# Optimization experiments

Measured on AMD Instinct MI355X. Metric: run time of the kernel, lower is better.

The kernel has to match this reference:

```python
import jax, jax.numpy as jnp
import numpy as np

N = 8192      # total nodes = B * NPG
D = 512       # in_dim = hidden_dim = out_dim
E = 131072    # edges
B = 16        # graphs (selected_idx batch)
NPG = 512     # nodes per graph
S = 128       # selected nodes per graph
L = 3         # conv layers
EPS = 1e-5


def setup_inputs() -> dict:
    key = jax.random.key(0)
    ks = jax.random.split(key, 16)
    scale = 0.02
    return {
        "x": jax.random.normal(ks[0], (N, D), dtype=jnp.float32),
        "edge_index": jax.random.randint(ks[1], (2, E), 0, N),
        "selected_idx": jax.random.randint(ks[2], (B, S), 0, NPG),
        "edge_label": jax.random.randint(ks[3], (E,), 0, 4),
        # per-layer EdgeConv MLP params (stacked over L layers)
        "conv_W1": jax.random.normal(ks[4], (L, 2 * D, D), dtype=jnp.float32) * scale,
        "conv_b1": jnp.full((L, D), 0.01, dtype=jnp.float32),
        "conv_W2": jax.random.normal(ks[5], (L, D, D), dtype=jnp.float32) * scale,
        "conv_b2": jnp.full((L, D), 0.01, dtype=jnp.float32),
        # shared layer norms
        "ln1_g": jnp.ones((D,), dtype=jnp.float32),
        "ln1_b": jnp.zeros((D,), dtype=jnp.float32),
        "ln2_g": jnp.ones((D,), dtype=jnp.float32),
        "ln2_b": jnp.zeros((D,), dtype=jnp.float32),
        # final FFN
        "ffn_W1": jax.random.normal(ks[6], (D, D), dtype=jnp.float32) * scale,
        "ffn_b1": jnp.full((D,), 0.01, dtype=jnp.float32),
        "ffn_W2": jax.random.normal(ks[7], (D, D), dtype=jnp.float32) * scale,
        "ffn_b2": jnp.full((D,), 0.01, dtype=jnp.float32),
    }


def _layer_norm(x, g, b):
    mu = jnp.mean(x, axis=-1, keepdims=True)
    var = jnp.mean(jnp.square(x - mu), axis=-1, keepdims=True)
    return (x - mu) * jax.lax.rsqrt(var + EPS) * g + b


def reference(x, edge_index, selected_idx, edge_label,
              conv_W1, conv_b1, conv_W2, conv_b2,
              ln1_g, ln1_b, ln2_g, ln2_b,
              ffn_W1, ffn_b1, ffn_W2, ffn_b2):
    src = edge_index[0]  # x_j source nodes
    dst = edge_index[1]  # x_i target nodes (aggregation index)
    for l in range(L):
        residual = x
        h = _layer_norm(x, ln1_g, ln1_b)
        hi = h[dst]                                   # [E, D]
        hj = h[src]                                   # [E, D]
        ef = jnp.concatenate([hi, hj - hi], axis=1)   # [E, 2D]
        m = jnp.maximum(ef @ conv_W1[l] + conv_b1[l], 0.0) @ conv_W2[l] + conv_b2[l]
        agg = jax.ops.segment_max(m, dst, num_segments=N)  # max-aggregate [N, D]
        agg = jnp.where(jnp.isfinite(agg), agg, 0.0)       # nodes w/o in-edges -> 0
        x = jnp.maximum(agg, 0.0) + residual
    residual = x
    h = _layer_norm(x, ln2_g, ln2_b)
    y = jnp.maximum(h @ ffn_W1 + ffn_b1, 0.0) @ ffn_W2 + ffn_b2
    x = y + residual
    x = x.reshape(B, NPG, D)
    idx = jnp.broadcast_to(selected_idx[:, :, None], (B, S, D))
    return jnp.take_along_axis(x, idx, axis=1)  # [B, S, D]
```

## Files before the change

### kernel.cpp

```cpp
#include <hip/hip_runtime.h>
#include <stdint.h>

#define NN 8192
#define DD 512
#define EE 131072
#define BBATCH 16
#define NPG 512
#define SSEL 128
#define LL 3

typedef unsigned short u16;
typedef __bf16 bf16x8 __attribute__((ext_vector_type(8)));
typedef float f32x4 __attribute__((ext_vector_type(4)));
typedef u16 u16x8 __attribute__((ext_vector_type(8)));

__device__ __forceinline__ float bf2f(u16 u) {
    union { unsigned i; float f; } v; v.i = ((unsigned)u) << 16; return v.f;
}
__device__ __forceinline__ u16 f2bf(float f) {
    union { unsigned i; float f; } v; v.f = f;
    unsigned i = v.i;
    return (u16)((i + 0x7FFFu + ((i >> 16) & 1u)) >> 16);
}

__device__ __forceinline__ void async_cp16(const u16* g, u16* l) {
    __builtin_amdgcn_global_load_lds(
        (const __attribute__((address_space(1))) unsigned int*)g,
        (__attribute__((address_space(3))) unsigned int*)l, 16, 0, 0);
}

__global__ __launch_bounds__(64) void ln_fused(const float* __restrict__ xin,
                                               float* __restrict__ agg_io,
                                               float* __restrict__ xout,
                                               const float* __restrict__ g,
                                               const float* __restrict__ b,
                                               u16* __restrict__ h, int doAdd) {
    int row = blockIdx.x;
    int lane = threadIdx.x;
    const f32x4* x4 = (const f32x4*)(xin + (size_t)row * DD);
    f32x4 p = x4[lane * 2], q = x4[lane * 2 + 1];
    if (doAdd) {
        const f32x4* a4 = (const f32x4*)(agg_io + (size_t)row * DD);
        f32x4 pa = a4[lane * 2], qa = a4[lane * 2 + 1];
        #pragma unroll
        for (int i = 0; i < 4; ++i) { p[i] += pa[i]; q[i] += qa[i]; }
    }
    if (agg_io) {
        f32x4 z;
        #pragma unroll
        for (int i = 0; i < 4; ++i) z[i] = 0.f;
        f32x4* a4 = (f32x4*)(agg_io + (size_t)row * DD);
        a4[lane * 2] = z;
        a4[lane * 2 + 1] = z;
    }
    f32x4* xo = (f32x4*)(xout + (size_t)row * DD);
    xo[lane * 2] = p;
    xo[lane * 2 + 1] = q;
    float v[8];
    v[0] = p[0]; v[1] = p[1]; v[2] = p[2]; v[3] = p[3];
    v[4] = q[0]; v[5] = q[1]; v[6] = q[2]; v[7] = q[3];
    float s = 0.f, sq = 0.f;
    #pragma unroll
    for (int i = 0; i < 8; ++i) { s += v[i]; sq += v[i] * v[i]; }
    #pragma unroll
    for (int o = 32; o >= 1; o >>= 1) { s += __shfl_xor(s, o); sq += __shfl_xor(sq, o); }
    float mu = s * (1.f / DD);
    float var = sq * (1.f / DD) - mu * mu;
    float rs = rsqrtf(var + 1e-5f);
    int kb = lane * 8;
    u16x8 o8;
    #pragma unroll
    for (int i = 0; i < 8; ++i) o8[i] = f2bf((v[i] - mu) * rs * g[kb + i] + b[kb + i]);
    *(u16x8*)(h + (size_t)row * DD + kb) = o8;
}

__global__ void hist_kernel(const int* __restrict__ dst, int* __restrict__ cnt) {
    int e = blockIdx.x * 256 + threadIdx.x;
    if (e < EE) atomicAdd(&cnt[dst[e]], 1);
}

__global__ __launch_bounds__(1024) void scan_kernel(const int* __restrict__ cnt,
                                                    int* __restrict__ off,
                                                    int* __restrict__ cur) {
    __shared__ int part[1024];
    int t = threadIdx.x;
    int base = t * 8;
    int loc[8]; int s = 0;
    #pragma unroll
    for (int i = 0; i < 8; ++i) { loc[i] = s; s += cnt[base + i]; }
    part[t] = s;
    __syncthreads();
    for (int o = 1; o < 1024; o <<= 1) {
        int v = part[t];
        int u = (t >= o) ? part[t - o] : 0;
        __syncthreads();
        part[t] = v + u;
        __syncthreads();
    }
    int bx = (t > 0) ? part[t - 1] : 0;
    #pragma unroll
    for (int i = 0; i < 8; ++i) { off[base + i] = bx + loc[i]; cur[base + i] = bx + loc[i]; }
    if (t == 0) off[NN] = part[1023];
}

__global__ void scatter_kernel(const int* __restrict__ src, const int* __restrict__ dst,
                               int* __restrict__ cur, int* __restrict__ ssrc,
                               int* __restrict__ sdst) {
    int e = blockIdx.x * 256 + threadIdx.x;
    if (e < EE) {
        int d = dst[e];
        int p = atomicAdd(&cur[d], 1);
        ssrc[p] = src[e];
        sdst[p] = d;
    }
}

__global__ __launch_bounds__(256) void cvt_t_kernel(const float* __restrict__ src,
                                                    u16* __restrict__ dstp, int K,
                                                    int Nn) {
    __shared__ u16 tile[32][33];
    int bk = blockIdx.x * 32, bn = blockIdx.y * 32;
    int tx = threadIdx.x & 31, ty = threadIdx.x >> 5;
    #pragma unroll
    for (int r = 0; r < 32; r += 8)
        tile[ty + r][tx] = f2bf(src[(size_t)(bk + ty + r) * Nn + bn + tx]);
    __syncthreads();
    #pragma unroll
    for (int r = 0; r < 32; r += 8)
        dstp[(size_t)(bn + ty + r) * K + bk + tx] = tile[tx][ty + r];
}

__global__ __launch_bounds__(256) void cvt_w1_kernel(const float* __restrict__ W1,
                                                     u16* __restrict__ dstp) {
    __shared__ u16 tile[32][33];
    int bk = blockIdx.x * 32, bn = blockIdx.y * 32;
    int tx = threadIdx.x & 31, ty = threadIdx.x >> 5;
    #pragma unroll
    for (int r = 0; r < 32; r += 8) {
        int k = bk + ty + r, n = bn + tx;
        float v = (n < 512) ? (W1[(size_t)k * 512 + n] - W1[(size_t)(k + 512) * 512 + n])
                            : W1[(size_t)(k + 512) * 512 + (n - 512)];
        tile[ty + r][tx] = f2bf(v);
    }
    __syncthreads();
    #pragma unroll
    for (int r = 0; r < 32; r += 8)
        dstp[(size_t)(bn + ty + r) * 512 + bk + tx] = tile[tx][ty + r];
}

template <int EMODE>
__global__ __launch_bounds__(256) void gemm_async(
    const u16* __restrict__ A, const u16* __restrict__ BT,
    const float* __restrict__ bias, const float* __restrict__ resid,
    void* __restrict__ Cout, int K, int ldc) {
    __shared__ u16 lA[128 * 64];
    __shared__ u16 lB[128 * 64];
    const int tid = threadIdx.x;
    const int lane = tid & 63, wave = tid >> 6;
    const int wm = wave & 1, wn = wave >> 1;
    const int quad = lane >> 4, lm = lane & 15;
    const int tileM = blockIdx.x, tileN = blockIdx.y;

    const int g = (lane & 7) ^ (lane >> 3);
    const u16* ap[4];
    const u16* bp[4];
    u16* lad[4];
    u16* lbd[4];
    #pragma unroll
    for (int j = 0; j < 4; ++j) {
        int seg = wave * 4 + j;
        int rA = tileM * 128 + seg * 8 + (lane >> 3);
        int rB = tileN * 128 + seg * 8 + (lane >> 3);
        ap[j] = A + (size_t)rA * K + g * 8;
        bp[j] = BT + (size_t)rB * K + g * 8;
        lad[j] = lA + seg * 512;
        lbd[j] = lB + seg * 512;
    }

    f32x4 acc[4][4];
    #pragma unroll
    for (int mt = 0; mt < 4; ++mt)
        #pragma unroll
        for (int nt = 0; nt < 4; ++nt)
            #pragma unroll
            for (int j = 0; j < 4; ++j) acc[mt][nt][j] = 0.f;

    for (int kb = 0; kb < K; kb += 64) {
        #pragma unroll
        for (int j = 0; j < 4; ++j) {
            async_cp16(ap[j], lad[j]);
            async_cp16(bp[j], lbd[j]);
            ap[j] += 64;
            bp[j] += 64;
        }
        __syncthreads();
        #pragma unroll
        for (int kk = 0; kk < 64; kk += 32) {
            bf16x8 af[4], bfr[4];
            int gbase = (kk >> 3) + quad;
            #pragma unroll
            for (int mt = 0; mt < 4; ++mt) {
                int row = wm * 64 + mt * 16 + lm;
                af[mt] = *(const bf16x8*)(lA + row * 64 + ((gbase ^ (row & 7)) << 3));
            }
            #pragma unroll
            for (int nt = 0; nt < 4; ++nt) {
                int row = wn * 64 + nt * 16 + lm;
                bfr[nt] = *(const bf16x8*)(lB + row * 64 + ((gbase ^ (row & 7)) << 3));
            }
            #pragma unroll
            for (int mt = 0; mt < 4; ++mt)
                #pragma unroll
                for (int nt = 0; nt < 4; ++nt)
                    acc[mt][nt] = __builtin_amdgcn_mfma_f32_16x16x32_bf16(
                        af[mt], bfr[nt], acc[mt][nt], 0, 0, 0);
        }
        __syncthreads();
    }
    #pragma unroll
    for (int mt = 0; mt < 4; ++mt) {
        #pragma unroll
        for (int nt = 0; nt < 4; ++nt) {
            int col = tileN * 128 + wn * 64 + nt * 16 + lm;
            float bv;
            if (EMODE == 2) bv = 0.f;
            else if (EMODE == 3) bv = (col < 512) ? bias[col] : 0.f;
            else bv = bias[col];
            #pragma unroll
            for (int j = 0; j < 4; ++j) {
                int grow = tileM * 128 + wm * 64 + mt * 16 + quad * 4 + j;
                float v = acc[mt][nt][j] + bv;
                if (EMODE == 0) {
                    ((u16*)Cout)[(size_t)grow * ldc + col] = f2bf(fmaxf(v, 0.f));
                } else if (EMODE == 1) {
                    ((float*)Cout)[(size_t)grow * ldc + col] =
                        v + resid[(size_t)grow * ldc + col];
                } else {
                    ((u16*)Cout)[(size_t)grow * ldc + col] = f2bf(v);
                }
            }
        }
    }
}

__global__ __launch_bounds__(512, 4) void gemm_edge(
    const u16* __restrict__ P, const int* __restrict__ ssrc,
    const int* __restrict__ sdst, const u16* __restrict__ W2T,
    const float* __restrict__ b2, float* __restrict__ agg) {
    __shared__ u16 smem[128 * 64 + 256 * 64];
    __shared__ int nid_l[128];
    u16* lA = smem;
    u16* lB = smem + 128 * 64;
    const int tid = threadIdx.x;
    const int lane = tid & 63, wave = tid >> 6;
    const int wm = wave & 1, wn = wave >> 1;
    const int quad = lane >> 4, lm = lane & 15;
    const int tileN = blockIdx.x;
    const int ebase = blockIdx.y * 128;

    if (tid < 128) nid_l[tid] = sdst[ebase + tid];

    const int g = (lane & 7) ^ (lane >> 3);
    int aoff[2], boff[2];
    u16* lout[2];
    #pragma unroll
    for (int j = 0; j < 2; ++j) {
        int seg = wave * 2 + j;
        int row = seg * 8 + (lane >> 3);
        int dn = sdst[ebase + row];
        int sn = ssrc[ebase + row];
        aoff[j] = dn * 1024 + g * 8;
        boff[j] = sn * 1024 + 512 + g * 8;
        lout[j] = lA + seg * 512 + lane * 8;
    }
    int woff[4];
    u16* lbd[4];
    #pragma unroll
    for (int j = 0; j < 4; ++j) {
        int seg = wave * 4 + j;
        int row = tileN * 256 + seg * 8 + (lane >> 3);
        woff[j] = row * 512 + g * 8;
        lbd[j] = lB + seg * 512;
    }

    f32x4 acc[4][4];
    #pragma unroll
    for (int mt = 0; mt < 4; ++mt)
        #pragma unroll
        for (int nt = 0; nt < 4; ++nt)
            #pragma unroll
            for (int j = 0; j < 4; ++j) acc[mt][nt][j] = 0.f;

    for (int kb = 0; kb < 512; kb += 64) {
        u16x8 ga[2], gb[2];
        #pragma unroll
        for (int j = 0; j < 2; ++j) {
            ga[j] = *(const u16x8*)(P + aoff[j] + kb);
            gb[j] = *(const u16x8*)(P + boff[j] + kb);
        }
        #pragma unroll
        for (int j = 0; j < 4; ++j) async_cp16(W2T + woff[j] + kb, lbd[j]);
        #pragma unroll
        for (int j = 0; j < 2; ++j) {
            union { u16x8 v; unsigned w[4]; } ua, ub;
            ua.v = ga[j];
            ub.v = gb[j];
            unsigned o[4];
            #pragma unroll
            for (int q = 0; q < 4; ++q) {
                float a0 = __uint_as_float(ua.w[q] << 16);
                float a1 = __uint_as_float(ua.w[q] & 0xffff0000u);
                float c0 = __uint_as_float(ub.w[q] << 16);
                float c1 = __uint_as_float(ub.w[q] & 0xffff0000u);
                float s0 = fmaxf(a0 + c0, 0.f);
                float s1 = fmaxf(a1 + c1, 0.f);
                unsigned r0 = __float_as_uint(s0) + 0x8000u;
                unsigned r1 = __float_as_uint(s1) + 0x8000u;
                o[q] = (r0 >> 16) | (r1 & 0xffff0000u);
            }
            *(uint4*)lout[j] = make_uint4(o[0], o[1], o[2], o[3]);
        }
        __syncthreads();
        #pragma unroll
        for (int kk = 0; kk < 64; kk += 32) {
            bf16x8 af[4], bfr[4];
            int gbase = (kk >> 3) + quad;
            #pragma unroll
            for (int mt = 0; mt < 4; ++mt) {
                int row = wm * 64 + mt * 16 + lm;
                af[mt] = *(const bf16x8*)(lA + row * 64 + ((gbase ^ (row & 7)) << 3));
            }
            #pragma unroll
            for (int nt = 0; nt < 4; ++nt) {
                int row = wn * 64 + nt * 16 + lm;
                bfr[nt] = *(const bf16x8*)(lB + row * 64 + ((gbase ^ (row & 7)) << 3));
            }
            #pragma unroll
            for (int mt = 0; mt < 4; ++mt)
                #pragma unroll
                for (int nt = 0; nt < 4; ++nt)
                    acc[mt][nt] = __builtin_amdgcn_mfma_f32_16x16x32_bf16(
                        af[mt], bfr[nt], acc[mt][nt], 0, 0, 0);
        }
        __syncthreads();
    }

    u16* cbuf = smem;
    for (int p = 0; p < 2; ++p) {
        if (wm == p) {
            #pragma unroll
            for (int nt = 0; nt < 4; ++nt) {
                int lcol = wn * 64 + nt * 16 + lm;
                float bv = b2[tileN * 256 + lcol];
                #pragma unroll
                for (int mt = 0; mt < 4; ++mt) {
                    #pragma unroll
                    for (int j2 = 0; j2 < 4; ++j2) {
                        int row = mt * 16 + quad * 4 + j2;
                        cbuf[row * 264 + lcol] = f2bf(fmaxf(acc[mt][nt][j2] + bv, 0.f));
                    }
                }
            }
        }
        __syncthreads();
        {
            int lcol = tid & 255;
            int gcol = tileN * 256 + lcol;
            int r0 = (tid >> 8) * 32;
            int gr0 = p * 64 + r0;
            int cur = nid_l[gr0];
            float run = bf2f(cbuf[r0 * 264 + lcol]);
            for (int r = 1; r < 32; ++r) {
                int nd = nid_l[gr0 + r];
                float v = bf2f(cbuf[(r0 + r) * 264 + lcol]);
                if (nd != cur) {
                    atomicMax((unsigned int*)&agg[(size_t)cur * DD + gcol],
                              __float_as_uint(run));
                    cur = nd;
                    run = v;
                } else {
                    run = fmaxf(run, v);
                }
            }
            atomicMax((unsigned int*)&agg[(size_t)cur * DD + gcol],
                      __float_as_uint(run));
        }
        __syncthreads();
    }
}

__global__ __launch_bounds__(128) void gather_fused(const float* __restrict__ x,
                                                    const float* __restrict__ agg,
                                                    const int* __restrict__ sel,
                                                    float* __restrict__ xs) {
    int i = blockIdx.x;
    int b = i >> 7;
    int r = b * NPG + sel[i];
    const f32x4* srcp = (const f32x4*)(x + (size_t)r * DD);
    const f32x4* aggp = (const f32x4*)(agg + (size_t)r * DD);
    f32x4 v = srcp[threadIdx.x];
    f32x4 a = aggp[threadIdx.x];
    #pragma unroll
    for (int j = 0; j < 4; ++j) v[j] += a[j];
    ((f32x4*)(xs + (size_t)i * DD))[threadIdx.x] = v;
}

extern "C" void kernel_launch(void* const* d_in, const int* in_sizes, int n_in,
                              void* d_out, int out_size, void* d_ws, size_t ws_size,
                              hipStream_t stream) {
    const float* x_in = (const float*)d_in[0];
    const int* ei = (const int*)d_in[1];
    const int* sel = (const int*)d_in[2];
    const float* W1 = (const float*)d_in[4];
    const float* b1 = (const float*)d_in[5];
    const float* W2 = (const float*)d_in[6];
    const float* b2 = (const float*)d_in[7];
    const float* g1 = (const float*)d_in[8];
    const float* be1 = (const float*)d_in[9];
    const float* g2 = (const float*)d_in[10];
    const float* be2 = (const float*)d_in[11];
    const float* fW1 = (const float*)d_in[12];
    const float* fb1 = (const float*)d_in[13];
    const float* fW2 = (const float*)d_in[14];
    const float* fb2 = (const float*)d_in[15];
    float* out = (float*)d_out;

    char* w = (char*)d_ws;
    size_t off = 0;
    auto alloc = [&](size_t bytes) -> char* {
        char* p = w + off;
        off += (bytes + 255) & ~(size_t)255;
        return p;
    };
    float* xbuf = (float*)alloc((size_t)NN * DD * 4);
    float* agg  = (float*)alloc((size_t)NN * DD * 4);
    u16* h      = (u16*)alloc((size_t)NN * DD * 2);
    u16* P      = (u16*)alloc((size_t)NN * 1024 * 2);
    u16* W1T    = (u16*)alloc((size_t)LL * 1024 * DD * 2);
    u16* W2T    = (u16*)alloc((size_t)LL * DD * DD * 2);
    u16* FW1T   = (u16*)alloc((size_t)DD * DD * 2);
    u16* FW2T   = (u16*)alloc((size_t)DD * DD * 2);
    int* cnt    = (int*)alloc((size_t)NN * 4);
    int* offs   = (int*)alloc((size_t)(NN + 1) * 4);
    int* cur    = (int*)alloc((size_t)NN * 4);
    int* ssrc   = (int*)alloc((size_t)EE * 4);
    int* sdst   = (int*)alloc((size_t)EE * 4);
    float* xs   = (float*)alloc((size_t)BBATCH * SSEL * DD * 4);
    u16* hs     = (u16*)alloc((size_t)BBATCH * SSEL * DD * 2);
    u16* uu     = (u16*)alloc((size_t)BBATCH * SSEL * DD * 2);

    const int* esrc = ei;
    const int* edst = ei + EE;

    hipMemsetAsync(cnt, 0, (size_t)NN * 4, stream);
    hist_kernel<<<EE / 256, 256, 0, stream>>>(edst, cnt);
    scan_kernel<<<1, 1024, 0, stream>>>(cnt, offs, cur);
    scatter_kernel<<<EE / 256, 256, 0, stream>>>(esrc, edst, cur, ssrc, sdst);

    for (int l = 0; l < LL; ++l) {
        cvt_w1_kernel<<<dim3(16, 32), 256, 0, stream>>>(
            W1 + (size_t)l * 1024 * DD, W1T + (size_t)l * 1024 * DD);
        cvt_t_kernel<<<dim3(16, 16), 256, 0, stream>>>(
            W2 + (size_t)l * DD * DD, W2T + (size_t)l * DD * DD, DD, DD);
    }
    cvt_t_kernel<<<dim3(16, 16), 256, 0, stream>>>(fW1, FW1T, DD, DD);
    cvt_t_kernel<<<dim3(16, 16), 256, 0, stream>>>(fW2, FW2T, DD, DD);

    for (int l = 0; l < LL; ++l) {
        ln_fused<<<NN, 64, 0, stream>>>(l == 0 ? x_in : xbuf, agg, xbuf, g1, be1, h,
                                        l > 0 ? 1 : 0);
        {
            dim3 grid(NN / 128, 1024 / 128);
            gemm_async<3><<<grid, 256, 0, stream>>>(
                h, W1T + (size_t)l * 1024 * DD, b1 + (size_t)l * DD, nullptr, P, DD,
                1024);
        }
        gemm_edge<<<dim3(2, EE / 128), 512, 0, stream>>>(
            P, ssrc, sdst, W2T + (size_t)l * DD * DD, b2 + (size_t)l * DD, agg);
    }

    gather_fused<<<BBATCH * SSEL, 128, 0, stream>>>(xbuf, agg, sel, xs);
    ln_fused<<<BBATCH * SSEL, 64, 0, stream>>>(xs, nullptr, xs, g2, be2, hs, 0);
    dim3 gridf(BBATCH * SSEL / 128, DD / 128);
    gemm_async<0><<<gridf, 256, 0, stream>>>(hs, FW1T, fb1, nullptr, uu, DD, DD);
    gemm_async<1><<<gridf, 256, 0, stream>>>(uu, FW2T, fb2, xs, out, DD, DD);
}
```

Before: 620.2 us.

## Batch weight conversions, pack four LN rows per block, use packed bf16 convert

Merges the per-layer weight transpose/convert launches into two launches, using blockIdx.z to index layers or jobs. Changes the layernorm kernel to process four rows per 256-thread block instead of one row per 64-thread block. Replaces the manual round-and-pack in the edge GEMM's relu prologue with a packed bf16 conversion builtin and vector max. Together these aim to cut launch overhead and ALU work. The packed builtin rounds to nearest-even, whereas the old code rounded half-up, so results may differ slightly.

```diff
diff --git a/kernel.cpp b/kernel.cpp
--- a/kernel.cpp
+++ b/kernel.cpp
@@ -12,6 +12,7 @@
 typedef unsigned short u16;
 typedef __bf16 bf16x8 __attribute__((ext_vector_type(8)));
 typedef float f32x4 __attribute__((ext_vector_type(4)));
+typedef float f32x2 __attribute__((ext_vector_type(2)));
 typedef u16 u16x8 __attribute__((ext_vector_type(8)));
 
 __device__ __forceinline__ float bf2f(u16 u) {
@@ -23,20 +24,35 @@
     return (u16)((i + 0x7FFFu + ((i >> 16) & 1u)) >> 16);
 }
 
+__device__ __forceinline__ unsigned pk_bf16(float s0, float s1) {
+#if __has_builtin(__builtin_amdgcn_cvt_pk_bf16_f32)
+    typedef __bf16 bf16x2 __attribute__((ext_vector_type(2)));
+    union { bf16x2 v; unsigned u; } r;
+    r.v = __builtin_amdgcn_cvt_pk_bf16_f32(s0, s1);
+    return r.u;
+#else
+    unsigned r0 = __float_as_uint(s0);
+    r0 = (r0 + 0x7FFFu + ((r0 >> 16) & 1u)) >> 16;
+    unsigned r1 = __float_as_uint(s1);
+    r1 = (r1 + 0x7FFFu + ((r1 >> 16) & 1u)) & 0xffff0000u;
+    return r0 | r1;
+#endif
+}
+
 __device__ __forceinline__ void async_cp16(const u16* g, u16* l) {
     __builtin_amdgcn_global_load_lds(
         (const __attribute__((address_space(1))) unsigned int*)g,
         (__attribute__((address_space(3))) unsigned int*)l, 16, 0, 0);
 }
 
-__global__ __launch_bounds__(64) void ln_fused(const float* __restrict__ xin,
-                                               float* __restrict__ agg_io,
-                                               float* __restrict__ xout,
-                                               const float* __restrict__ g,
-                                               const float* __restrict__ b,
-                                               u16* __restrict__ h, int doAdd) {
-    int row = blockIdx.x;
-    int lane = threadIdx.x;
+__global__ __launch_bounds__(256) void ln_fused(const float* __restrict__ xin,
+                                                float* __restrict__ agg_io,
+                                                float* __restrict__ xout,
+                                                const float* __restrict__ g,
+                                                const float* __restrict__ b,
+                                                u16* __restrict__ h, int doAdd) {
+    int row = blockIdx.x * 4 + (threadIdx.x >> 6);
+    int lane = threadIdx.x & 63;
     const f32x4* x4 = (const f32x4*)(xin + (size_t)row * DD);
     f32x4 p = x4[lane * 2], q = x4[lane * 2 + 1];
     if (doAdd) {
@@ -115,24 +131,30 @@
     }
 }
 
-__global__ __launch_bounds__(256) void cvt_t_kernel(const float* __restrict__ src,
-                                                    u16* __restrict__ dstp, int K,
-                                                    int Nn) {
+struct CvtJobs {
+    const float* s[5];
+    u16* d[5];
+};
+__global__ __launch_bounds__(256) void cvt_t5_kernel(CvtJobs jobs) {
     __shared__ u16 tile[32][33];
+    const float* src = jobs.s[blockIdx.z];
+    u16* dstp = jobs.d[blockIdx.z];
     int bk = blockIdx.x * 32, bn = blockIdx.y * 32;
     int tx = threadIdx.x & 31, ty = threadIdx.x >> 5;
     #pragma unroll
     for (int r = 0; r < 32; r += 8)
-        tile[ty + r][tx] = f2bf(src[(size_t)(bk + ty + r) * Nn + bn + tx]);
+        tile[ty + r][tx] = f2bf(src[(size_t)(bk + ty + r) * 512 + bn + tx]);
     __syncthreads();
     #pragma unroll
     for (int r = 0; r < 32; r += 8)
-        dstp[(size_t)(bn + ty + r) * K + bk + tx] = tile[tx][ty + r];
-}
-
-__global__ __launch_bounds__(256) void cvt_w1_kernel(const float* __restrict__ W1,
-                                                     u16* __restrict__ dstp) {
+        dstp[(size_t)(bn + ty + r) * 512 + bk + tx] = tile[tx][ty + r];
+}
+
+__global__ __launch_bounds__(256) void cvt_w1_kernel(const float* __restrict__ W1g,
+                                                     u16* __restrict__ dstg) {
     __shared__ u16 tile[32][33];
+    const float* W1 = W1g + (size_t)blockIdx.z * 1024 * 512;
+    u16* dstp = dstg + (size_t)blockIdx.z * 1024 * 512;
     int bk = blockIdx.x * 32, bn = blockIdx.y * 32;
     int tx = threadIdx.x & 31, ty = threadIdx.x >> 5;
     #pragma unroll
@@ -308,15 +330,20 @@
             unsigned o[4];
             #pragma unroll
             for (int q = 0; q < 4; ++q) {
-                float a0 = __uint_as_float(ua.w[q] << 16);
-                float a1 = __uint_as_float(ua.w[q] & 0xffff0000u);
-                float c0 = __uint_as_float(ub.w[q] << 16);
-                float c1 = __uint_as_float(ub.w[q] & 0xffff0000u);
-                float s0 = fmaxf(a0 + c0, 0.f);
-                float s1 = fmaxf(a1 + c1, 0.f);
-                unsigned r0 = __float_as_uint(s0) + 0x8000u;
-                unsigned r1 = __float_as_uint(s1) + 0x8000u;
-                o[q] = (r0 >> 16) | (r1 & 0xffff0000u);
+                f32x2 a, c;
+                a[0] = __uint_as_float(ua.w[q] << 16);
+                a[1] = __uint_as_float(ua.w[q] & 0xffff0000u);
+                c[0] = __uint_as_float(ub.w[q] << 16);
+                c[1] = __uint_as_float(ub.w[q] & 0xffff0000u);
+                f32x2 s = a + c;
+#if __has_builtin(__builtin_elementwise_max)
+                f32x2 z; z[0] = 0.f; z[1] = 0.f;
+                s = __builtin_elementwise_max(s, z);
+#else
+                s[0] = fmaxf(s[0], 0.f);
+                s[1] = fmaxf(s[1], 0.f);
+#endif
+                o[q] = pk_bf16(s[0], s[1]);
             }
             *(uint4*)lout[j] = make_uint4(o[0], o[1], o[2], o[3]);
         }
@@ -457,18 +484,25 @@
     scan_kernel<<<1, 1024, 0, stream>>>(cnt, offs, cur);
     scatter_kernel<<<EE / 256, 256, 0, stream>>>(esrc, edst, cur, ssrc, sdst);
 
+    cvt_w1_kernel<<<dim3(16, 32, LL), 256, 0, stream>>>(W1, W1T);
+    {
+        CvtJobs jobs;
+        jobs.s[0] = W2;
+        jobs.s[1] = W2 + (size_t)DD * DD;
+        jobs.s[2] = W2 + (size_t)2 * DD * DD;
+        jobs.s[3] = fW1;
+        jobs.s[4] = fW2;
+        jobs.d[0] = W2T;
+        jobs.d[1] = W2T + (size_t)DD * DD;
+        jobs.d[2] = W2T + (size_t)2 * DD * DD;
+        jobs.d[3] = FW1T;
+        jobs.d[4] = FW2T;
+        cvt_t5_kernel<<<dim3(16, 16, 5), 256, 0, stream>>>(jobs);
+    }
+
     for (int l = 0; l < LL; ++l) {
-        cvt_w1_kernel<<<dim3(16, 32), 256, 0, stream>>>(
-            W1 + (size_t)l * 1024 * DD, W1T + (size_t)l * 1024 * DD);
-        cvt_t_kernel<<<dim3(16, 16), 256, 0, stream>>>(
-            W2 + (size_t)l * DD * DD, W2T + (size_t)l * DD * DD, DD, DD);
-    }
-    cvt_t_kernel<<<dim3(16, 16), 256, 0, stream>>>(fW1, FW1T, DD, DD);
-    cvt_t_kernel<<<dim3(16, 16), 256, 0, stream>>>(fW2, FW2T, DD, DD);
-
-    for (int l = 0; l < LL; ++l) {
-        ln_fused<<<NN, 64, 0, stream>>>(l == 0 ? x_in : xbuf, agg, xbuf, g1, be1, h,
-                                        l > 0 ? 1 : 0);
+        ln_fused<<<NN / 4, 256, 0, stream>>>(l == 0 ? x_in : xbuf, agg, xbuf, g1, be1,
+                                             h, l > 0 ? 1 : 0);
         {
             dim3 grid(NN / 128, 1024 / 128);
             gemm_async<3><<<grid, 256, 0, stream>>>(
@@ -480,7 +514,7 @@
     }
 
     gather_fused<<<BBATCH * SSEL, 128, 0, stream>>>(xbuf, agg, sel, xs);
-    ln_fused<<<BBATCH * SSEL, 64, 0, stream>>>(xs, nullptr, xs, g2, be2, hs, 0);
+    ln_fused<<<BBATCH * SSEL / 4, 256, 0, stream>>>(xs, nullptr, xs, g2, be2, hs, 0);
     dim3 gridf(BBATCH * SSEL / 128, DD / 128);
     gemm_async<0><<<gridf, 256, 0, stream>>>(hs, FW1T, fb1, nullptr, uu, DD, DD);
     gemm_async<1><<<gridf, 256, 0, stream>>>(uu, FW2T, fb2, xs, out, DD, DD);
```

Result: faster. 548.4 us (-11.6%).
